# Kernel tuning notes

Hardware: AMD Instinct MI355X
Metric: run time of the kernel (lower is better)

The kernel has to match this reference:

```python
import jax, jax.numpy as jnp
import numpy as np

B, T, D = 32, 2048, 256   # batch, encoder time steps, input_dim
H = 256                   # output_dim (GRU hidden)
A = 128                   # attention_dim
C = 4367                  # nb_classes
STEPS = 22                # max_out_t_steps


def setup_inputs() -> dict:
    key = jax.random.key(0)
    ks = jax.random.split(key, 11)
    s = 0.05
    return {
        "x": jax.random.normal(ks[0], (B, T, D), dtype=jnp.float32),
        # additive attention params: softmax_T(tanh(x Wx + h Wh) @ v)
        "Wx": jax.random.normal(ks[1], (D, A), dtype=jnp.float32) * s,
        "Wh": jax.random.normal(ks[2], (H, A), dtype=jnp.float32) * s,
        "v": jax.random.normal(ks[3], (A,), dtype=jnp.float32) * s,
        # torch GRUCell params
        "W_ih": jax.random.normal(ks[4], (3 * H, D), dtype=jnp.float32) * s,
        "W_hh": jax.random.normal(ks[5], (3 * H, H), dtype=jnp.float32) * s,
        "b_ih": jax.random.normal(ks[6], (3 * H,), dtype=jnp.float32) * s,
        "b_hh": jax.random.normal(ks[7], (3 * H,), dtype=jnp.float32) * s,
        # classifier
        "W_cls": jax.random.normal(ks[8], (C, H), dtype=jnp.float32) * s,
        "b_cls": jax.random.normal(ks[9], (C,), dtype=jnp.float32) * s,
    }


def reference(x, Wx, Wh, v, W_ih, W_hh, b_ih, b_hh, W_cls, b_cls):
    # dropout layers are identity in eval/reference mode
    xW = jnp.einsum("btd,da->bta", x, Wx)  # hoisted: constant across steps
    h0 = jnp.zeros((x.shape[0], H), dtype=x.dtype)

    def step(h, _):
        # additive attention over time axis
        e = jnp.einsum("bta,a->bt", jnp.tanh(xW + (h @ Wh)[:, None, :]), v)
        att = jax.nn.softmax(e, axis=1)          # [B, T]
        ctx = jnp.einsum("btd,bt->bd", x, att)   # weighted sum over T
        # torch GRUCell
        gi = ctx @ W_ih.T + b_ih                  # [B, 3H]
        gh = h @ W_hh.T + b_hh                    # [B, 3H]
        i_r, i_z, i_n = jnp.split(gi, 3, axis=1)
        h_r, h_z, h_n = jnp.split(gh, 3, axis=1)
        r = jax.nn.sigmoid(i_r + h_r)
        z = jax.nn.sigmoid(i_z + h_z)
        n = jnp.tanh(i_n + r * h_n)
        h_new = (1.0 - z) * n + z * h
        logits = h_new @ W_cls.T + b_cls          # [B, C]
        return h_new, logits

    _, outs = jax.lax.scan(step, h0, None, length=STEPS)  # [STEPS, B, C]
    return jnp.transpose(outs, (1, 0, 2))                 # [B, STEPS, C]
```

## Files before the change

### kernel.cpp

```cpp
#include <hip/hip_runtime.h>

#define BB 32
#define TT 2048
#define DD 256
#define HH 256
#define AA 128
#define CC 4367
#define CLS_LD 4480
#define NSTEPS 22
#define NCHUNK 32

typedef unsigned short ushortT;
typedef unsigned int uintT;
typedef unsigned long long u64T;
using frag8 = __attribute__((ext_vector_type(8))) short;
using f32x4 = __attribute__((ext_vector_type(4))) float;

__device__ __forceinline__ float tanh_fast(float u) {
  float e = __expf(2.0f * u);
  return 1.0f - 2.0f / (e + 1.0f);
}
__device__ __forceinline__ float sigmoid_fast(float u) {
  return 1.0f / (1.0f + __expf(-u));
}
__device__ __forceinline__ ushortT f2bf(float f) {
  unsigned int u = __float_as_uint(f);
  unsigned int r = (u + 0x7FFFu + ((u >> 16) & 1u)) >> 16;
  return (ushortT)r;
}
__device__ __forceinline__ float bf2f(ushortT v) {
  return __uint_as_float(((unsigned int)v) << 16);
}

__global__ __launch_bounds__(256) void trans_kernel(
    const float* __restrict__ Wx, const float* __restrict__ W_cls,
    float* __restrict__ WclsT, ushortT* __restrict__ WxT_bf) {
  int blk = blockIdx.x;
  __shared__ float tile[32][33];
  const int li = threadIdx.x >> 5, lj = threadIdx.x & 31;
  if (blk < 1096) {
    int i0 = (blk >> 3) * 32, j0 = (blk & 7) * 32;
#pragma unroll
    for (int k = 0; k < 4; ++k) {
      int i = i0 + li + k * 8;
      if (i < CC) tile[li + k * 8][lj] = W_cls[(size_t)i * 256 + j0 + lj];
    }
    __syncthreads();
#pragma unroll
    for (int k = 0; k < 4; ++k) {
      int j = j0 + li + k * 8, i = i0 + lj;
      if (i < CC) WclsT[(size_t)j * CLS_LD + i] = tile[lj][li + k * 8];
    }
  } else {
    blk -= 1096;
    int i0 = (blk >> 2) * 32, j0 = (blk & 3) * 32;
#pragma unroll
    for (int k = 0; k < 4; ++k)
      tile[li + k * 8][lj] = Wx[(size_t)(i0 + li + k * 8) * 128 + j0 + lj];
    __syncthreads();
#pragma unroll
    for (int k = 0; k < 4; ++k) {
      int j = j0 + li + k * 8;
      WxT_bf[(size_t)j * 256 + i0 + lj] = f2bf(tile[lj][li + k * 8]);
    }
  }
}

__global__ __launch_bounds__(256) void xw_mfma(
    const float* __restrict__ x, const ushortT* __restrict__ WxT_bf,
    ushortT* __restrict__ x_bf, ushortT* __restrict__ xWT) {
  __shared__ ushortT lds[2 * 128 * 72];
#define SX(r, c) lds[(r) * 72 + (c)]
#define SW(r, c) lds[128 * 72 + (r) * 72 + (c)]
#define ST(a, m) lds[(a) * 136 + (m)]
  const int tid = threadIdx.x;
  const int lane = tid & 63, w = tid >> 6;
  const int l15 = lane & 15, quad = lane >> 4;
  const int r0 = blockIdx.x * 128;
  const int bb = blockIdx.x >> 4, t0 = (blockIdx.x & 15) * 128;
  const int row = tid >> 1, half = tid & 1;

  f32x4 acc[2][8];
#pragma unroll
  for (int mt = 0; mt < 2; ++mt)
#pragma unroll
    for (int nt = 0; nt < 8; ++nt) acc[mt][nt] = (f32x4){0.f, 0.f, 0.f, 0.f};

  for (int kk0 = 0; kk0 < 256; kk0 += 64) {
    {
      const float4* xp = (const float4*)(x + (size_t)(r0 + row) * DD + kk0 + half * 32);
      uint4 pk[4];
#pragma unroll
      for (int i = 0; i < 4; ++i) {
        float4 f0 = xp[2 * i], f1 = xp[2 * i + 1];
        pk[i].x = (uintT)f2bf(f0.x) | ((uintT)f2bf(f0.y) << 16);
        pk[i].y = (uintT)f2bf(f0.z) | ((uintT)f2bf(f0.w) << 16);
        pk[i].z = (uintT)f2bf(f1.x) | ((uintT)f2bf(f1.y) << 16);
        pk[i].w = (uintT)f2bf(f1.z) | ((uintT)f2bf(f1.w) << 16);
      }
      uint4* sxp = (uint4*)&SX(row, half * 32);
      uint4* gxp = (uint4*)(x_bf + (size_t)(r0 + row) * DD + kk0 + half * 32);
#pragma unroll
      for (int i = 0; i < 4; ++i) { sxp[i] = pk[i]; gxp[i] = pk[i]; }
    }
    {
      const uint4* wp = (const uint4*)(WxT_bf + (size_t)row * DD + kk0 + half * 32);
      uint4* swp = (uint4*)&SW(row, half * 32);
#pragma unroll
      for (int i = 0; i < 4; ++i) swp[i] = wp[i];
    }
    __syncthreads();
#pragma unroll
    for (int kk = 0; kk < 2; ++kk) {
      frag8 a0 = *(const frag8*)&SX(w * 32 + l15, kk * 32 + quad * 8);
      frag8 a1 = *(const frag8*)&SX(w * 32 + 16 + l15, kk * 32 + quad * 8);
#pragma unroll
      for (int nt = 0; nt < 8; ++nt) {
        frag8 bf = *(const frag8*)&SW(nt * 16 + l15, kk * 32 + quad * 8);
        acc[0][nt] = __builtin_amdgcn_mfma_f32_16x16x32_bf16(a0, bf, acc[0][nt], 0, 0, 0);
        acc[1][nt] = __builtin_amdgcn_mfma_f32_16x16x32_bf16(a1, bf, acc[1][nt], 0, 0, 0);
      }
    }
    __syncthreads();
  }
#pragma unroll
  for (int mt = 0; mt < 2; ++mt)
#pragma unroll
    for (int nt = 0; nt < 8; ++nt)
#pragma unroll
      for (int r = 0; r < 4; ++r) {
        int m = w * 32 + mt * 16 + quad * 4 + r;
        int a = nt * 16 + l15;
        ST(a, m) = f2bf(acc[mt][nt][r]);
      }
  __syncthreads();
  {
    const uint4* sp = (const uint4*)&ST(row, half * 64);
    uint4* gp = (uint4*)(xWT + ((size_t)bb * AA + row) * TT + t0 + half * 64);
#pragma unroll
    for (int i = 0; i < 8; ++i) gp[i] = sp[i];
  }
#undef SX
#undef SW
#undef ST
}

__global__ __launch_bounds__(256) void gates_kernel(
    const float* __restrict__ ctx_part, const float* __restrict__ den_part,
    const float* __restrict__ hall, const float* __restrict__ W_ih,
    const float* __restrict__ W_hh, const float* __restrict__ b_ih,
    const float* __restrict__ b_hh, float* __restrict__ gi_buf,
    float* __restrict__ gh_buf, int s) {
  const int slice = blockIdx.x, b = blockIdx.y, tid = threadIdx.x;
  __shared__ __align__(16) float sctx[DD];
  __shared__ float sden;
  if (tid < 32) {
    float d = den_part[b * NCHUNK + tid];
#pragma unroll
    for (int off = 16; off > 0; off >>= 1) d += __shfl_down(d, off, 32);
    if (tid == 0) sden = d;
  }
  {
    float acc = 0.f;
#pragma unroll
    for (int c = 0; c < NCHUNK; ++c)
      acc += ctx_part[((size_t)b * NCHUNK + c) * DD + tid];
    sctx[tid] = acc;
  }
  __syncthreads();
  const float invd = 1.0f / sden;
  const int kq = tid & 15, gsub = tid >> 4;
  const float4* cp = (const float4*)sctx + kq * 4;
  const float4* hrow = (s >= 2) ? (const float4*)(hall + ((size_t)(s - 2) * BB + b) * HH) + kq * 4 : nullptr;
  float4 c4[4], h4[4];
#pragma unroll
  for (int j = 0; j < 4; ++j) {
    float4 cv = cp[j];
    c4[j].x = cv.x * invd; c4[j].y = cv.y * invd; c4[j].z = cv.z * invd; c4[j].w = cv.w * invd;
    if (hrow) h4[j] = hrow[j];
    else { h4[j].x = 0.f; h4[j].y = 0.f; h4[j].z = 0.f; h4[j].w = 0.f; }
  }
#pragma unroll
  for (int it = 0; it < 3; ++it) {
    const int g = slice * 48 + it * 16 + gsub;
    const float4* wi = (const float4*)(W_ih + (size_t)g * DD) + kq * 4;
    const float4* wh = (const float4*)(W_hh + (size_t)g * HH) + kq * 4;
    float gi = 0.f, gh = 0.f;
#pragma unroll
    for (int j = 0; j < 4; ++j) {
      float4 wv = wi[j];
      gi += c4[j].x * wv.x + c4[j].y * wv.y + c4[j].z * wv.z + c4[j].w * wv.w;
      wv = wh[j];
      gh += h4[j].x * wv.x + h4[j].y * wv.y + h4[j].z * wv.z + h4[j].w * wv.w;
    }
#pragma unroll
    for (int off = 8; off > 0; off >>= 1) {
      gi += __shfl_down(gi, off, 16);
      gh += __shfl_down(gh, off, 16);
    }
    if (kq == 0) {
      gi_buf[b * 768 + g] = gi + b_ih[g];
      gh_buf[b * 768 + g] = gh + b_hh[g];
    }
  }
}

__global__ __launch_bounds__(256) void hcomb_kernel(
    const float* __restrict__ gi_buf, const float* __restrict__ gh_buf,
    const float* __restrict__ Wh, float* __restrict__ hall,
    float* __restrict__ hWh_buf, int s) {
  const int b = blockIdx.x, as = blockIdx.y, i = threadIdx.x;
  __shared__ float sh[HH];
  __shared__ float part[8][32];
  {
    float gir = gi_buf[b * 768 + i], giz = gi_buf[b * 768 + 256 + i], gin = gi_buf[b * 768 + 512 + i];
    float ghr = gh_buf[b * 768 + i], ghz = gh_buf[b * 768 + 256 + i], ghn = gh_buf[b * 768 + 512 + i];
    float hp = (s >= 2) ? hall[((size_t)(s - 2) * BB + b) * HH + i] : 0.f;
    float r = sigmoid_fast(gir + ghr);
    float z = sigmoid_fast(giz + ghz);
    float n = tanh_fast(gin + r * ghn);
    float hv = (1.f - z) * n + z * hp;
    if (as == 0) hall[((size_t)(s - 1) * BB + b) * HH + i] = hv;
    sh[i] = hv;
  }
  __syncthreads();
  {
    const int a = i & 31, kq = i >> 5;
    const int ga = as * 32 + a;
    float acc = 0.f;
#pragma unroll
    for (int k = kq * 32; k < kq * 32 + 32; ++k)
      acc = fmaf(sh[k], Wh[k * AA + ga], acc);
    part[kq][a] = acc;
  }
  __syncthreads();
  if (i < 32) {
    float sum = part[0][i] + part[1][i] + part[2][i] + part[3][i]
              + part[4][i] + part[5][i] + part[6][i] + part[7][i];
    hWh_buf[b * AA + as * 32 + i] = sum;
  }
}

__global__ __launch_bounds__(256, 4) void att_kernel(
    const ushortT* __restrict__ x_bf, const ushortT* __restrict__ xWT_bf,
    const float* __restrict__ hWh_buf, const float* __restrict__ v,
    float* __restrict__ ctx_part, float* __restrict__ den_part) {
  const int tid = threadIdx.x;
  const int b = blockIdx.x;
  const int chunk = blockIdx.y;
  const int t0 = chunk * 64;
  __shared__ float sh_hWh[AA], sh_v[AA];
  __shared__ float sh_part[8 * 64];
  __shared__ float sh_w[64];
  __shared__ __align__(16) float sh_ctx[4 * DD];
  if (tid < AA) {
    sh_hWh[tid] = hWh_buf ? hWh_buf[b * AA + tid] : 0.f;
    sh_v[tid] = v[tid];
  }
  __syncthreads();
  const int j4 = tid >> 6, dq = tid & 63;
  u64T xr[16];
  {
    const u64T* xb4 = (const u64T*)x_bf;
#pragma unroll
    for (int j = 0; j < 16; ++j)
      xr[j] = __builtin_nontemporal_load(
          &xb4[(((size_t)(b * TT + t0 + j * 4 + j4)) * DD >> 2) + dq]);
  }
  {
    const int q = tid >> 5, tp = tid & 31;
    float p0 = 0.f, p1 = 0.f;
    const ushort2* xw2 = (const ushort2*)xWT_bf;
    const size_t base = (size_t)b * (AA * TT / 2) + (t0 >> 1) + tp;
#pragma unroll
    for (int i = 0; i < 16; ++i) {
      int a = q * 16 + i;
      ushort2 u = xw2[base + (size_t)a * (TT / 2)];
      float hwa = sh_hWh[a], va = sh_v[a];
      p0 = fmaf(tanh_fast(bf2f(u.x) + hwa), va, p0);
      p1 = fmaf(tanh_fast(bf2f(u.y) + hwa), va, p1);
    }
    sh_part[q * 64 + 2 * tp] = p0;
    sh_part[q * 64 + 2 * tp + 1] = p1;
  }
  __syncthreads();
  if (tid < 64) {
    float e = 0.f;
#pragma unroll
    for (int q = 0; q < 8; ++q) e += sh_part[q * 64 + tid];
    sh_w[tid] = __expf(e);
  }
  __syncthreads();
  {
    float4 acc = {0.f, 0.f, 0.f, 0.f};
#pragma unroll
    for (int j = 0; j < 16; ++j) {
      float w = sh_w[j * 4 + j4];
      u64T u = xr[j];
      acc.x = fmaf(w, bf2f((ushortT)(u       & 0xFFFFu)), acc.x);
      acc.y = fmaf(w, bf2f((ushortT)((u >> 16) & 0xFFFFu)), acc.y);
      acc.z = fmaf(w, bf2f((ushortT)((u >> 32) & 0xFFFFu)), acc.z);
      acc.w = fmaf(w, bf2f((ushortT)((u >> 48) & 0xFFFFu)), acc.w);
    }
    ((float4*)sh_ctx)[j4 * 64 + dq] = acc;
  }
  __syncthreads();
  {
    float sum = sh_ctx[tid] + sh_ctx[DD + tid] + sh_ctx[2 * DD + tid] + sh_ctx[3 * DD + tid];
    ctx_part[((size_t)b * NCHUNK + chunk) * DD + tid] = sum;
  }
  if (tid < 64) {
    float ds = sh_w[tid];
#pragma unroll
    for (int off = 32; off > 0; off >>= 1) ds += __shfl_down(ds, off, 64);
    if (tid == 0) den_part[b * NCHUNK + chunk] = ds;
  }
}

__global__ __launch_bounds__(256) void cls_kernel(
    const float* __restrict__ hall, const float* __restrict__ WclsT,
    const float* __restrict__ b_cls, float* __restrict__ out) {
  const int tid = threadIdx.x;
  const int c0 = blockIdx.x * 128;
  const int r0 = blockIdx.y * 32;
  const int cq = tid & 31, rg = tid >> 5;
  const int c = c0 + cq * 4;
  __shared__ __align__(16) float shh[32 * HH];
  {
    const float4* hsrc = (const float4*)(hall + (size_t)r0 * HH);
    float4* hdst = (float4*)shh;
#pragma unroll
    for (int i = 0; i < 8; ++i) hdst[tid + 256 * i] = hsrc[tid + 256 * i];
  }
  __syncthreads();
  float acc[4][4];
#pragma unroll
  for (int j = 0; j < 4; ++j)
#pragma unroll
    for (int l = 0; l < 4; ++l) acc[j][l] = 0.f;
#pragma unroll 4
  for (int k = 0; k < HH; ++k) {
    float4 w4 = *(const float4*)(WclsT + (size_t)k * CLS_LD + c);
    float h0 = shh[(rg * 4 + 0) * HH + k];
    float h1 = shh[(rg * 4 + 1) * HH + k];
    float h2 = shh[(rg * 4 + 2) * HH + k];
    float h3 = shh[(rg * 4 + 3) * HH + k];
    acc[0][0] = fmaf(h0, w4.x, acc[0][0]); acc[0][1] = fmaf(h0, w4.y, acc[0][1]);
    acc[0][2] = fmaf(h0, w4.z, acc[0][2]); acc[0][3] = fmaf(h0, w4.w, acc[0][3]);
    acc[1][0] = fmaf(h1, w4.x, acc[1][0]); acc[1][1] = fmaf(h1, w4.y, acc[1][1]);
    acc[1][2] = fmaf(h1, w4.z, acc[1][2]); acc[1][3] = fmaf(h1, w4.w, acc[1][3]);
    acc[2][0] = fmaf(h2, w4.x, acc[2][0]); acc[2][1] = fmaf(h2, w4.y, acc[2][1]);
    acc[2][2] = fmaf(h2, w4.z, acc[2][2]); acc[2][3] = fmaf(h2, w4.w, acc[2][3]);
    acc[3][0] = fmaf(h3, w4.x, acc[3][0]); acc[3][1] = fmaf(h3, w4.y, acc[3][1]);
    acc[3][2] = fmaf(h3, w4.z, acc[3][2]); acc[3][3] = fmaf(h3, w4.w, acc[3][3]);
  }
#pragma unroll
  for (int j = 0; j < 4; ++j) {
    int row = r0 + rg * 4 + j;
    int bb = row & (BB - 1), st = row >> 5;
    size_t obase = ((size_t)bb * NSTEPS + st) * CC;
#pragma unroll
    for (int l = 0; l < 4; ++l) {
      int cc = c + l;
      if (cc < CC) out[obase + cc] = acc[j][l] + b_cls[cc];
    }
  }
}

extern "C" void kernel_launch(void* const* d_in, const int* in_sizes, int n_in,
                              void* d_out, int out_size, void* d_ws, size_t ws_size,
                              hipStream_t stream) {
  const float* x     = (const float*)d_in[0];
  const float* Wx    = (const float*)d_in[1];
  const float* Wh    = (const float*)d_in[2];
  const float* v     = (const float*)d_in[3];
  const float* W_ih  = (const float*)d_in[4];
  const float* W_hh  = (const float*)d_in[5];
  const float* b_ih  = (const float*)d_in[6];
  const float* b_hh  = (const float*)d_in[7];
  const float* W_cls = (const float*)d_in[8];
  const float* b_cls = (const float*)d_in[9];
  float* out = (float*)d_out;

  float* ctx_part = (float*)d_ws;
  float* den_part = ctx_part + (size_t)BB * NCHUNK * DD;
  float* hWh_buf  = den_part + BB * NCHUNK;
  float* gi_buf   = hWh_buf + BB * AA;
  float* gh_buf   = gi_buf + BB * 768;
  float* hall     = gh_buf + BB * 768;
  float* WclsT    = hall + (size_t)NSTEPS * BB * HH;
  ushortT* WxT_bf = (ushortT*)(WclsT + (size_t)256 * CLS_LD);
  ushortT* x_bf   = WxT_bf + 128 * 256;
  ushortT* xWT    = x_bf + (size_t)BB * TT * DD;

  trans_kernel<<<1096 + 32, 256, 0, stream>>>(Wx, W_cls, WclsT, WxT_bf);
  xw_mfma<<<(BB * TT) / 128, 256, 0, stream>>>(x, WxT_bf, x_bf, xWT);

  att_kernel<<<dim3(BB, NCHUNK), 256, 0, stream>>>(x_bf, xWT, nullptr, v, ctx_part, den_part);
  for (int s = 1; s < NSTEPS; ++s) {
    gates_kernel<<<dim3(16, BB), 256, 0, stream>>>(ctx_part, den_part, hall, W_ih, W_hh,
                                                   b_ih, b_hh, gi_buf, gh_buf, s);
    hcomb_kernel<<<dim3(BB, 4), 256, 0, stream>>>(gi_buf, gh_buf, Wh, hall, hWh_buf, s);
    att_kernel<<<dim3(BB, NCHUNK), 256, 0, stream>>>(x_bf, xWT, hWh_buf, v, ctx_part, den_part);
  }
  gates_kernel<<<dim3(16, BB), 256, 0, stream>>>(ctx_part, den_part, hall, W_ih, W_hh,
                                                 b_ih, b_hh, gi_buf, gh_buf, NSTEPS);
  hcomb_kernel<<<dim3(BB, 4), 256, 0, stream>>>(gi_buf, gh_buf, Wh, hall, hWh_buf, NSTEPS);
  cls_kernel<<<dim3(35, 22), 256, 0, stream>>>(hall, WclsT, b_cls, out);
}
```

Baseline: 636.4 us.

## Fuse GRU combine and hWh projection into gates kernel via last-block counter

The separate hcomb kernel is removed. The last of the 16 gate-slice blocks for each batch row (found with an atomic counter) now computes the GRU update, writes h, and projects it through Wh to produce hWh. This saves 22 kernel launches and their inter-kernel gaps on the serial recurrence. In exchange, the Wh projection for each batch row runs in a single block instead of four, and correctness depends on threadfence and atomic ordering plus a memset of the counters.

Result: slower. 1.681 ms (+164.2%).

```diff
diff --git a/kernel.cpp b/kernel.cpp
--- a/kernel.cpp
+++ b/kernel.cpp
@@ -147,13 +147,18 @@
 
 __global__ __launch_bounds__(256) void gates_kernel(
     const float* __restrict__ ctx_part, const float* __restrict__ den_part,
-    const float* __restrict__ hall, const float* __restrict__ W_ih,
+    const float* __restrict__ hall_c, const float* __restrict__ W_ih,
     const float* __restrict__ W_hh, const float* __restrict__ b_ih,
-    const float* __restrict__ b_hh, float* __restrict__ gi_buf,
-    float* __restrict__ gh_buf, int s) {
+    const float* __restrict__ b_hh, const float* __restrict__ Wh,
+    float* __restrict__ gi_buf, float* __restrict__ gh_buf,
+    float* __restrict__ hall, float* __restrict__ hWh_buf,
+    uintT* __restrict__ g_cnt, int s) {
   const int slice = blockIdx.x, b = blockIdx.y, tid = threadIdx.x;
   __shared__ __align__(16) float sctx[DD];
   __shared__ float sden;
+  __shared__ float sh[HH];
+  __shared__ float part[2][AA];
+  __shared__ int sflag;
   if (tid < 32) {
     float d = den_part[b * NCHUNK + tid];
 #pragma unroll
@@ -171,7 +176,7 @@
   const float invd = 1.0f / sden;
   const int kq = tid & 15, gsub = tid >> 4;
   const float4* cp = (const float4*)sctx + kq * 4;
-  const float4* hrow = (s >= 2) ? (const float4*)(hall + ((size_t)(s - 2) * BB + b) * HH) + kq * 4 : nullptr;
+  const float4* hrow = (s >= 2) ? (const float4*)(hall_c + ((size_t)(s - 2) * BB + b) * HH) + kq * 4 : nullptr;
   float4 c4[4], h4[4];
 #pragma unroll
   for (int j = 0; j < 4; ++j) {
@@ -203,41 +208,40 @@
       gh_buf[b * 768 + g] = gh + b_hh[g];
     }
   }
-}
-
-__global__ __launch_bounds__(256) void hcomb_kernel(
-    const float* __restrict__ gi_buf, const float* __restrict__ gh_buf,
-    const float* __restrict__ Wh, float* __restrict__ hall,
-    float* __restrict__ hWh_buf, int s) {
-  const int b = blockIdx.x, as = blockIdx.y, i = threadIdx.x;
-  __shared__ float sh[HH];
-  __shared__ float part[8][32];
-  {
-    float gir = gi_buf[b * 768 + i], giz = gi_buf[b * 768 + 256 + i], gin = gi_buf[b * 768 + 512 + i];
-    float ghr = gh_buf[b * 768 + i], ghz = gh_buf[b * 768 + 256 + i], ghn = gh_buf[b * 768 + 512 + i];
-    float hp = (s >= 2) ? hall[((size_t)(s - 2) * BB + b) * HH + i] : 0.f;
+  __threadfence();
+  __syncthreads();
+  if (tid == 0) {
+    uintT old = __hip_atomic_fetch_add(&g_cnt[b], 1u, __ATOMIC_ACQ_REL,
+                                       __HIP_MEMORY_SCOPE_AGENT);
+    sflag = ((old & 15u) == 15u) ? 1 : 0;
+  }
+  __syncthreads();
+  if (sflag) {
+    __threadfence();
+    float gir = gi_buf[b * 768 + tid];
+    float giz = gi_buf[b * 768 + 256 + tid];
+    float gin = gi_buf[b * 768 + 512 + tid];
+    float ghr = gh_buf[b * 768 + tid];
+    float ghz = gh_buf[b * 768 + 256 + tid];
+    float ghn = gh_buf[b * 768 + 512 + tid];
+    float hp = (s >= 2) ? hall_c[((size_t)(s - 2) * BB + b) * HH + tid] : 0.f;
     float r = sigmoid_fast(gir + ghr);
     float z = sigmoid_fast(giz + ghz);
     float n = tanh_fast(gin + r * ghn);
     float hv = (1.f - z) * n + z * hp;
-    if (as == 0) hall[((size_t)(s - 1) * BB + b) * HH + i] = hv;
-    sh[i] = hv;
-  }
-  __syncthreads();
-  {
-    const int a = i & 31, kq = i >> 5;
-    const int ga = as * 32 + a;
-    float acc = 0.f;
-#pragma unroll
-    for (int k = kq * 32; k < kq * 32 + 32; ++k)
-      acc = fmaf(sh[k], Wh[k * AA + ga], acc);
-    part[kq][a] = acc;
-  }
-  __syncthreads();
-  if (i < 32) {
-    float sum = part[0][i] + part[1][i] + part[2][i] + part[3][i]
-              + part[4][i] + part[5][i] + part[6][i] + part[7][i];
-    hWh_buf[b * AA + as * 32 + i] = sum;
+    hall[((size_t)(s - 1) * BB + b) * HH + tid] = hv;
+    sh[tid] = hv;
+    __syncthreads();
+    {
+      const int a = tid & 127, kh = tid >> 7;
+      float acc = 0.f;
+#pragma unroll 8
+      for (int k = kh * 128; k < kh * 128 + 128; ++k)
+        acc = fmaf(sh[k], Wh[k * AA + a], acc);
+      part[kh][a] = acc;
+    }
+    __syncthreads();
+    if (tid < AA) hWh_buf[b * AA + tid] = part[0][tid] + part[1][tid];
   }
 }
 
@@ -382,7 +386,8 @@
   const float* b_cls = (const float*)d_in[9];
   float* out = (float*)d_out;
 
-  float* ctx_part = (float*)d_ws;
+  uintT* g_cnt    = (uintT*)d_ws;
+  float* ctx_part = (float*)d_ws + 256;
   float* den_part = ctx_part + (size_t)BB * NCHUNK * DD;
   float* hWh_buf  = den_part + BB * NCHUNK;
   float* gi_buf   = hWh_buf + BB * AA;
@@ -393,18 +398,17 @@
   ushortT* x_bf   = WxT_bf + 128 * 256;
   ushortT* xWT    = x_bf + (size_t)BB * TT * DD;
 
+  hipMemsetAsync(g_cnt, 0, 256 * sizeof(uintT), stream);
   trans_kernel<<<1096 + 32, 256, 0, stream>>>(Wx, W_cls, WclsT, WxT_bf);
   xw_mfma<<<(BB * TT) / 128, 256, 0, stream>>>(x, WxT_bf, x_bf, xWT);
 
   att_kernel<<<dim3(BB, NCHUNK), 256, 0, stream>>>(x_bf, xWT, nullptr, v, ctx_part, den_part);
-  for (int s = 1; s < NSTEPS; ++s) {
+  for (int s = 1; s <= NSTEPS; ++s) {
     gates_kernel<<<dim3(16, BB), 256, 0, stream>>>(ctx_part, den_part, hall, W_ih, W_hh,
-                                                   b_ih, b_hh, gi_buf, gh_buf, s);
-    hcomb_kernel<<<dim3(BB, 4), 256, 0, stream>>>(gi_buf, gh_buf, Wh, hall, hWh_buf, s);
-    att_kernel<<<dim3(BB, NCHUNK), 256, 0, stream>>>(x_bf, xWT, hWh_buf, v, ctx_part, den_part);
-  }
-  gates_kernel<<<dim3(16, BB), 256, 0, stream>>>(ctx_part, den_part, hall, W_ih, W_hh,
-                                                 b_ih, b_hh, gi_buf, gh_buf, NSTEPS);
-  hcomb_kernel<<<dim3(BB, 4), 256, 0, stream>>>(gi_buf, gh_buf, Wh, hall, hWh_buf, NSTEPS);
+                                                   b_ih, b_hh, Wh, gi_buf, gh_buf,
+                                                   hall, hWh_buf, g_cnt, s);
+    if (s < NSTEPS)
+      att_kernel<<<dim3(BB, NCHUNK), 256, 0, stream>>>(x_bf, xWT, hWh_buf, v, ctx_part, den_part);
+  }
   cls_kernel<<<dim3(35, 22), 256, 0, stream>>>(hall, WclsT, b_cls, out);
 }
```

## Store xW time-major and reduce attention scores with quad shuffles

Applied to the files above, without the earlier changes.

The precomputed xW is now stored as [B*T, A] rows instead of transposed [B, A, T]. Each attention thread loads 32 contiguous bf16 values with wide uint4 loads and reduces across 4 lanes with shuffles. This replaces the scattered 4-byte strided loads, the shared partial buffer and one barrier. Adjacent lanes now touch scattered LDS addresses for hWh and v, and the global loads are strided by row, which may change coalescing.

After: 632.4 us. No clear change (-0.6%).

```diff
diff --git a/kernel.cpp b/kernel.cpp
--- a/kernel.cpp
+++ b/kernel.cpp
@@ -68,16 +68,15 @@
 
 __global__ __launch_bounds__(256) void xw_mfma(
     const float* __restrict__ x, const ushortT* __restrict__ WxT_bf,
-    ushortT* __restrict__ x_bf, ushortT* __restrict__ xWT) {
+    ushortT* __restrict__ x_bf, ushortT* __restrict__ xW_ta) {
   __shared__ ushortT lds[2 * 128 * 72];
 #define SX(r, c) lds[(r) * 72 + (c)]
 #define SW(r, c) lds[128 * 72 + (r) * 72 + (c)]
-#define ST(a, m) lds[(a) * 136 + (m)]
+#define ST(m, a) lds[(m) * 136 + (a)]
   const int tid = threadIdx.x;
   const int lane = tid & 63, w = tid >> 6;
   const int l15 = lane & 15, quad = lane >> 4;
   const int r0 = blockIdx.x * 128;
-  const int bb = blockIdx.x >> 4, t0 = (blockIdx.x & 15) * 128;
   const int row = tid >> 1, half = tid & 1;
 
   f32x4 acc[2][8];
@@ -131,12 +130,12 @@
       for (int r = 0; r < 4; ++r) {
         int m = w * 32 + mt * 16 + quad * 4 + r;
         int a = nt * 16 + l15;
-        ST(a, m) = f2bf(acc[mt][nt][r]);
+        ST(m, a) = f2bf(acc[mt][nt][r]);
       }
   __syncthreads();
   {
     const uint4* sp = (const uint4*)&ST(row, half * 64);
-    uint4* gp = (uint4*)(xWT + ((size_t)bb * AA + row) * TT + t0 + half * 64);
+    uint4* gp = (uint4*)(xW_ta + (size_t)(r0 + row) * AA + half * 64);
 #pragma unroll
     for (int i = 0; i < 8; ++i) gp[i] = sp[i];
   }
@@ -242,7 +241,7 @@
 }
 
 __global__ __launch_bounds__(256, 4) void att_kernel(
-    const ushortT* __restrict__ x_bf, const ushortT* __restrict__ xWT_bf,
+    const ushortT* __restrict__ x_bf, const ushortT* __restrict__ xW_ta,
     const float* __restrict__ hWh_buf, const float* __restrict__ v,
     float* __restrict__ ctx_part, float* __restrict__ den_part) {
   const int tid = threadIdx.x;
@@ -250,7 +249,6 @@
   const int chunk = blockIdx.y;
   const int t0 = chunk * 64;
   __shared__ float sh_hWh[AA], sh_v[AA];
-  __shared__ float sh_part[8 * 64];
   __shared__ float sh_w[64];
   __shared__ __align__(16) float sh_ctx[4 * DD];
   if (tid < AA) {
@@ -268,27 +266,25 @@
           &xb4[(((size_t)(b * TT + t0 + j * 4 + j4)) * DD >> 2) + dq]);
   }
   {
-    const int q = tid >> 5, tp = tid & 31;
-    float p0 = 0.f, p1 = 0.f;
-    const ushort2* xw2 = (const ushort2*)xWT_bf;
-    const size_t base = (size_t)b * (AA * TT / 2) + (t0 >> 1) + tp;
-#pragma unroll
-    for (int i = 0; i < 16; ++i) {
-      int a = q * 16 + i;
-      ushort2 u = xw2[base + (size_t)a * (TT / 2)];
-      float hwa = sh_hWh[a], va = sh_v[a];
-      p0 = fmaf(tanh_fast(bf2f(u.x) + hwa), va, p0);
-      p1 = fmaf(tanh_fast(bf2f(u.y) + hwa), va, p1);
-    }
-    sh_part[q * 64 + 2 * tp] = p0;
-    sh_part[q * 64 + 2 * tp + 1] = p1;
-  }
-  __syncthreads();
-  if (tid < 64) {
+    const int tl = tid >> 2, aseg = tid & 3;
+    const uint4* xw16 = (const uint4*)(xW_ta + (size_t)(b * TT + t0 + tl) * AA + aseg * 32);
     float e = 0.f;
 #pragma unroll
-    for (int q = 0; q < 8; ++q) e += sh_part[q * 64 + tid];
-    sh_w[tid] = __expf(e);
+    for (int i = 0; i < 4; ++i) {
+      uint4 u = xw16[i];
+      const int ab = aseg * 32 + i * 8;
+      e = fmaf(tanh_fast(bf2f((ushortT)(u.x & 0xFFFFu)) + sh_hWh[ab + 0]), sh_v[ab + 0], e);
+      e = fmaf(tanh_fast(bf2f((ushortT)(u.x >> 16)) + sh_hWh[ab + 1]), sh_v[ab + 1], e);
+      e = fmaf(tanh_fast(bf2f((ushortT)(u.y & 0xFFFFu)) + sh_hWh[ab + 2]), sh_v[ab + 2], e);
+      e = fmaf(tanh_fast(bf2f((ushortT)(u.y >> 16)) + sh_hWh[ab + 3]), sh_v[ab + 3], e);
+      e = fmaf(tanh_fast(bf2f((ushortT)(u.z & 0xFFFFu)) + sh_hWh[ab + 4]), sh_v[ab + 4], e);
+      e = fmaf(tanh_fast(bf2f((ushortT)(u.z >> 16)) + sh_hWh[ab + 5]), sh_v[ab + 5], e);
+      e = fmaf(tanh_fast(bf2f((ushortT)(u.w & 0xFFFFu)) + sh_hWh[ab + 6]), sh_v[ab + 6], e);
+      e = fmaf(tanh_fast(bf2f((ushortT)(u.w >> 16)) + sh_hWh[ab + 7]), sh_v[ab + 7], e);
+    }
+    e += __shfl_xor(e, 1, 4);
+    e += __shfl_xor(e, 2, 4);
+    if (aseg == 0) sh_w[tl] = __expf(e);
   }
   __syncthreads();
   {
@@ -391,17 +387,17 @@
   float* WclsT    = hall + (size_t)NSTEPS * BB * HH;
   ushortT* WxT_bf = (ushortT*)(WclsT + (size_t)256 * CLS_LD);
   ushortT* x_bf   = WxT_bf + 128 * 256;
-  ushortT* xWT    = x_bf + (size_t)BB * TT * DD;
+  ushortT* xW_ta  = x_bf + (size_t)BB * TT * DD;
 
   trans_kernel<<<1096 + 32, 256, 0, stream>>>(Wx, W_cls, WclsT, WxT_bf);
-  xw_mfma<<<(BB * TT) / 128, 256, 0, stream>>>(x, WxT_bf, x_bf, xWT);
-
-  att_kernel<<<dim3(BB, NCHUNK), 256, 0, stream>>>(x_bf, xWT, nullptr, v, ctx_part, den_part);
+  xw_mfma<<<(BB * TT) / 128, 256, 0, stream>>>(x, WxT_bf, x_bf, xW_ta);
+
+  att_kernel<<<dim3(BB, NCHUNK), 256, 0, stream>>>(x_bf, xW_ta, nullptr, v, ctx_part, den_part);
   for (int s = 1; s < NSTEPS; ++s) {
     gates_kernel<<<dim3(16, BB), 256, 0, stream>>>(ctx_part, den_part, hall, W_ih, W_hh,
                                                    b_ih, b_hh, gi_buf, gh_buf, s);
     hcomb_kernel<<<dim3(BB, 4), 256, 0, stream>>>(gi_buf, gh_buf, Wh, hall, hWh_buf, s);
-    att_kernel<<<dim3(BB, NCHUNK), 256, 0, stream>>>(x_bf, xWT, hWh_buf, v, ctx_part, den_part);
+    att_kernel<<<dim3(BB, NCHUNK), 256, 0, stream>>>(x_bf, xW_ta, hWh_buf, v, ctx_part, den_part);
   }
   gates_kernel<<<dim3(16, BB), 256, 0, stream>>>(ctx_part, den_part, hall, W_ih, W_hh,
                                                  b_ih, b_hh, gi_buf, gh_buf, NSTEPS);
```
